# Performance work log

Measured on AMD Instinct MI355X. Metric: run time of the kernel, lower is better.

## Reference

```python
import jax, jax.numpy as jnp
import numpy as np

K, N, M, P, H = 8, 16, 8, 32, 32
BSZ, T = 128, 512
TAU = 0.5
P_STAY = 0.9


def setup_inputs() -> dict:
    key = jax.random.key(0)
    ks = jax.random.split(key, 20)
    f32 = jnp.float32
    norm = lambda k, s, sc=1.0: (jax.random.normal(k, s) * sc).astype(f32)
    sw = 1.0 / np.sqrt(H)  # torch GRU init scale
    return {
        "a_seq": norm(ks[0], (BSZ, T, P)),
        "A": norm(ks[1], (K, N, N), 0.1),
        "Bmat": norm(ks[2], (K, N, M), 0.1),
        "C": norm(ks[3], (K, P, N), 0.1),
        "Q": (jnp.tile(jnp.eye(N, dtype=f32)[None], (K, 1, 1)) + norm(ks[4], (K, N, N), 0.01)),
        "wih_f": norm(ks[5], (3 * H, P), sw),
        "whh_f": norm(ks[6], (3 * H, H), sw),
        "bih_f": norm(ks[7], (3 * H,), sw),
        "bhh_f": norm(ks[8], (3 * H,), sw),
        "wih_b": norm(ks[9], (3 * H, P), sw),
        "whh_b": norm(ks[10], (3 * H, H), sw),
        "bih_b": norm(ks[11], (3 * H,), sw),
        "bhh_b": norm(ks[12], (3 * H,), sw),
        "wl": norm(ks[13], (K * K, 2 * H), sw),
        "bl": norm(ks[14], (K * K,), sw),
        "wi": norm(ks[15], (K, 2 * H), sw),
        "bi": norm(ks[16], (K,), sw),
        "u0": jax.random.uniform(ks[17], (BSZ, K), minval=1e-6, maxval=1.0 - 1e-6, dtype=f32),
        "useq": jax.random.uniform(ks[18], (BSZ, T - 1, K), minval=1e-6, maxval=1.0 - 1e-6, dtype=f32),
    }


def _gru_dir(gx, whh, bhh, reverse):
    # gx: [T, B, 3H] precomputed input-to-hidden gates; torch GRU cell math
    def step(h, g):
        gh = h @ whh.T + bhh
        xr, xz, xn = jnp.split(g, 3, axis=-1)
        hr, hz, hn = jnp.split(gh, 3, axis=-1)
        r = jax.nn.sigmoid(xr + hr)
        z = jax.nn.sigmoid(xz + hz)
        n = jnp.tanh(xn + r * hn)
        h_new = (1.0 - z) * n + z * h
        return h_new, h_new
    h0 = jnp.zeros((gx.shape[1], whh.shape[1]), gx.dtype)
    _, hs = jax.lax.scan(step, h0, gx, reverse=reverse)
    return hs  # [T, B, H]


def reference(a_seq, A, Bmat, C, Q, wih_f, whh_f, bih_f, bhh_f,
              wih_b, whh_b, bih_b, bhh_b, wl, bl, wi, bi, u0, useq):
    Bn, Tn, _ = a_seq.shape
    Kn = A.shape[0]
    x = a_seq.transpose(1, 0, 2)  # [T, B, P]
    hf = _gru_dir(x @ wih_f.T + bih_f, whh_f, bhh_f, False)
    hb = _gru_dir(x @ wih_b.T + bih_b, whh_b, bhh_b, True)
    h_seq = jnp.concatenate([hf, hb], axis=-1)  # [T, B, 2H]

    logits = (h_seq @ wl.T + bl).reshape(Tn, Bn, Kn, Kn)  # [T, B, K, K]
    init_logits = h_seq[0] @ wi.T + bi                     # [B, K]

    g0 = -jnp.log(-jnp.log(u0))
    gseq = -jnp.log(-jnp.log(useq))  # [B, T-1, K]

    # t = 0 (soft gumbel-softmax since is_training=True)
    y0 = jax.nn.softmax((init_logits + g0) / TAU, axis=-1)
    lq0 = (y0 * jax.nn.log_softmax(init_logits, axis=-1)).sum(-1)
    lp0 = (y0 * jnp.log(1.0 / Kn)).sum(-1)  # torch: full_like(1/K).log()

    trans = jnp.full((Kn, Kn), (1.0 - P_STAY) / (Kn - 1), a_seq.dtype)
    trans = trans.at[jnp.arange(Kn), jnp.arange(Kn)].set(P_STAY)

    def step(y_prev, xs):
        lg, g = xs  # lg: [B, K, K], g: [B, K]
        l_t = jnp.einsum('bk,bkj->bj', y_prev, lg)
        y_t = jax.nn.softmax((l_t + g) / TAU, axis=-1)
        lq = (y_t * jax.nn.log_softmax(l_t, axis=-1)).sum(-1)
        tp = y_prev @ trans
        lp = (y_t * jnp.log(jnp.clip(tp, 1e-8))).sum(-1)
        return y_t, (y_t, lq, lp)

    _, (ys, lqs, lps) = jax.lax.scan(step, y0, (logits[1:], gseq.transpose(1, 0, 2)))

    y_seq = jnp.concatenate([y0[None], ys], axis=0).transpose(1, 0, 2)  # [B, T, K]
    log_qseq = jnp.concatenate([lq0[None], lqs], axis=0).T              # [B, T]
    log_pseq = jnp.concatenate([lp0[None], lps], axis=0).T              # [B, T]

    A_seq = jnp.einsum('btk,kij->btij', y_seq, A)
    B_seq = jnp.einsum('btk,knm->btnm', y_seq, Bmat)
    Q_seq = jnp.einsum('btk,kij->btij', y_seq, Q)
    C_seq = jnp.broadcast_to(C[0], (Bn, Tn) + C[0].shape)
    return (A_seq, B_seq, C_seq, Q_seq, log_qseq, log_pseq)
```

## Files before the change

kernel.cpp:

```cpp
#include <hip/hip_runtime.h>
#include <math.h>

#define T 512
#define B 128
#define KK 8
#define HH 32
#define PP 32

#define WS_GX    0
#define WS_GS    6291456
#define WS_HSEQ  12582912
#define WS_LOGITS 0
#define WS_INIT  16777216
#define WS_YSEQ  16778240

#define OUT_A    0
#define OUT_B    16777216
#define OUT_C    25165824
#define OUT_Q    58720256
#define OUT_LQ   75497472
#define OUT_LP   75563008

#define TINV 2.0f
#define PSTAY 0.9f
#define OFFV (0.1f / 7.0f)
#define DPS (PSTAY - OFFV)
#define LOG_INV_K (-2.0794415416798357f)

typedef float f4v __attribute__((ext_vector_type(4)));
typedef __attribute__((address_space(3))) float as3f;

__device__ __forceinline__ void dma16(unsigned ldsbyte, int voffbyte, const void* sbase) {
    asm volatile("s_mov_b32 m0, %0\n\t"
                 "global_load_lds_dwordx4 %1, %2"
                 :: "s"(ldsbyte), "v"(voffbyte), "s"(sbase)
                 : "memory");
}
__device__ __forceinline__ void st16(void* p, f4v v) {
    asm volatile("global_store_dwordx4 %0, %1, off" :: "v"(p), "v"(v) : "memory");
}
__device__ __forceinline__ f4v ldsr16(int addr) {
    f4v out;
    asm volatile("ds_read_b128 %0, %1" : "=v"(out) : "v"(addr));
    return out;
}
__device__ __forceinline__ f4v ldg16(const void* p) {
    f4v out;
    asm volatile("global_load_dwordx4 %0, %1, off" : "=v"(out) : "v"(p) : "memory");
    return out;
}
__device__ __forceinline__ float ldg4(const void* p) {
    float out;
    asm volatile("global_load_dword %0, %1, off" : "=v"(out) : "v"(p) : "memory");
    return out;
}

__global__ __launch_bounds__(192) void gx_kernel(
    const float* __restrict__ a_seq,
    const float* __restrict__ wih_f, const float* __restrict__ bih_f,
    const float* __restrict__ wih_b, const float* __restrict__ bih_b,
    float* __restrict__ gx) {
    __shared__ float xt[64 * 32];
    int blk = blockIdx.x;
    int b = blk >> 3;
    int t0 = (blk & 7) << 6;
    int g = threadIdx.x;
    int dir = (g >= 96) ? 1 : 0;
    int gg = dir ? (g - 96) : g;
    const float* w = dir ? wih_b : wih_f;
    const float* bv = dir ? bih_b : bih_f;

    {
        const float4* src = (const float4*)(a_seq + ((size_t)b * T + t0) * PP);
        float4* dst = (float4*)xt;
        for (int idx = g; idx < 512; idx += 192) dst[idx] = src[idx];
    }
    float wreg[32];
#pragma unroll
    for (int q = 0; q < 8; ++q) {
        float4 wv = *(const float4*)(w + (size_t)gg * PP + q * 4);
        wreg[q * 4 + 0] = wv.x; wreg[q * 4 + 1] = wv.y;
        wreg[q * 4 + 2] = wv.z; wreg[q * 4 + 3] = wv.w;
    }
    float bias = bv[gg];
    __syncthreads();

    float* op = gx + ((size_t)(dir * B + b) * T + t0) * 96 + gg;
#pragma unroll 4
    for (int r = 0; r < 64; ++r) {
        const float4* xr = (const float4*)(xt + r * 32);
        float acc = bias;
#pragma unroll
        for (int q = 0; q < 8; ++q) {
            float4 xv = xr[q];
            acc = fmaf(xv.x, wreg[q * 4 + 0], acc);
            acc = fmaf(xv.y, wreg[q * 4 + 1], acc);
            acc = fmaf(xv.z, wreg[q * 4 + 2], acc);
            acc = fmaf(xv.w, wreg[q * 4 + 3], acc);
        }
        op[(size_t)r * 96] = acc;
    }
}

__global__ __launch_bounds__(64, 1) void gru_kernel(
    const float* __restrict__ gx,
    const float* __restrict__ whh_f, const float* __restrict__ bhh_f,
    const float* __restrict__ whh_b, const float* __restrict__ bhh_b,
    float* __restrict__ hseq) {
    int cid = blockIdx.x;
    int b = cid & 127;
    int dir = cid >> 7;
    int i = threadIdx.x & 31;
    const float* whh = dir ? whh_b : whh_f;
    const float* bhh = dir ? bhh_b : bhh_f;
    const float* gp0 = gx + (size_t)cid * (T * 96);

    f4v wr[8], wz[8], wn[8];
#pragma unroll
    for (int q = 0; q < 8; ++q) {
        wr[q] = ldg16(whh + (size_t)i * 32 + q * 4);
        wz[q] = ldg16(whh + (size_t)(32 + i) * 32 + q * 4);
        wn[q] = ldg16(whh + (size_t)(64 + i) * 32 + q * 4);
    }
    float bhr = ldg4(bhh + i);
    float bhz = ldg4(bhh + 32 + i);
    float bhn = ldg4(bhh + 64 + i);

    const float* p = gp0 + (dir ? (T - 1) * 96 : 0);
    int gstep = dir ? -96 : 96;
    int voff = (((dir ? (T - 1) : 0) * B + b) * 64 + dir * 32 + i) * 4;
    int vstep = dir ? -(B * 64 * 4) : (B * 64 * 4);

    float pxrA[8], pxzA[8], pxnA[8], pxrB[8], pxzB[8], pxnB[8];

#define LOADG(PR, PZ, PN, G0) do {                                             \
        _Pragma("unroll")                                                      \
        for (int u_ = 0; u_ < 8; ++u_) {                                       \
            int sc_ = (G0) * 8 + u_; if (sc_ > T - 1) sc_ = T - 1;             \
            const float* rp_ = p + sc_ * gstep;                                \
            PR[u_] = ldg4(rp_ + i);                                            \
            PZ[u_] = ldg4(rp_ + 32 + i);                                       \
            PN[u_] = ldg4(rp_ + 64 + i);                                       \
        }                                                                      \
    } while (0)

#define GWAIT(N) do {                                                          \
        asm volatile("s_waitcnt vmcnt(" #N ")" ::: "memory");                  \
        __builtin_amdgcn_sched_barrier(0);                                     \
    } while (0)

#define GSTEP(PR, PZ, PN, SLOT) do {                                           \
        float hr_ = PR[SLOT] + bhr;                                            \
        float hz_ = PZ[SLOT] + bhz;                                            \
        float hn_ = bhn;                                                       \
        _Pragma("unroll")                                                      \
        for (int q_ = 0; q_ < 8; ++q_) {                                       \
            _Pragma("unroll")                                                  \
            for (int c_ = 0; c_ < 4; ++c_) {                                   \
                float hj_ = __uint_as_float(                                   \
                    __builtin_amdgcn_readlane(__float_as_uint(h), q_ * 4 + c_)); \
                hr_ = fmaf(wr[q_][c_], hj_, hr_);                              \
                hz_ = fmaf(wz[q_][c_], hj_, hz_);                              \
                hn_ = fmaf(wn[q_][c_], hj_, hn_);                              \
            }                                                                  \
        }                                                                      \
        float r_ = __builtin_amdgcn_rcpf(1.f + __expf(-hr_));                  \
        float z_ = __builtin_amdgcn_rcpf(1.f + __expf(-hz_));                  \
        float na_ = fmaf(r_, hn_, PN[SLOT]);                                   \
        float e2_ = __expf(-2.f * fabsf(na_));                                 \
        float n_ = copysignf((1.f - e2_) * __builtin_amdgcn_rcpf(1.f + e2_), na_); \
        h = fmaf(z_, h - n_, n_);                                              \
        asm volatile("global_store_dword %0, %1, %2"                           \
                     :: "v"(voff), "v"(h), "s"(hseq) : "memory");              \
        voff += vstep;                                                         \
    } while (0)

    LOADG(pxrA, pxzA, pxnA, 0);
    GWAIT(0);
    float h = 0.f;

    for (int gq = 0; gq < 32; ++gq) {
        LOADG(pxrB, pxzB, pxnB, 2 * gq + 1);
        GWAIT(32);
        GSTEP(pxrA, pxzA, pxnA, 0); GSTEP(pxrA, pxzA, pxnA, 1);
        GSTEP(pxrA, pxzA, pxnA, 2); GSTEP(pxrA, pxzA, pxnA, 3);
        GSTEP(pxrA, pxzA, pxnA, 4); GSTEP(pxrA, pxzA, pxnA, 5);
        GSTEP(pxrA, pxzA, pxnA, 6); GSTEP(pxrA, pxzA, pxnA, 7);
        LOADG(pxrA, pxzA, pxnA, 2 * gq + 2);
        GWAIT(32);
        GSTEP(pxrB, pxzB, pxnB, 0); GSTEP(pxrB, pxzB, pxnB, 1);
        GSTEP(pxrB, pxzB, pxnB, 2); GSTEP(pxrB, pxzB, pxnB, 3);
        GSTEP(pxrB, pxzB, pxnB, 4); GSTEP(pxrB, pxzB, pxnB, 5);
        GSTEP(pxrB, pxzB, pxnB, 6); GSTEP(pxrB, pxzB, pxnB, 7);
    }
#undef LOADG
#undef GWAIT
#undef GSTEP
}

__global__ __launch_bounds__(256) void logits_kernel(
    const float* __restrict__ hseq,
    const float* __restrict__ wl, const float* __restrict__ bl,
    const float* __restrict__ wi, const float* __restrict__ bi,
    float* __restrict__ logits, float* __restrict__ initl) {
    __shared__ float wls[64 * 65];
    __shared__ float hrow[4][64];
    int tid = threadIdx.x;
    for (int i2 = tid; i2 < 1024; i2 += 256) {
        float4 v = ((const float4*)wl)[i2];
        int gr = i2 >> 4;
        int cc = (i2 & 15) * 4;
        float* d = &wls[gr * 65 + cc];
        d[0] = v.x; d[1] = v.y; d[2] = v.z; d[3] = v.w;
    }
    int q = tid >> 6;
    int tb = blockIdx.x * 4 + q;
    int g = tid & 63;
    hrow[q][g] = hseq[(size_t)tb * 64 + g];
    __syncthreads();
    float acc = bl[g];
    const float* wrow = &wls[g * 65];
#pragma unroll
    for (int c = 0; c < 64; ++c) acc = fmaf(wrow[c], hrow[q][c], acc);
    logits[(size_t)tb * 64 + g] = acc * TINV;
    if (tb < B && g < 8) {
        float a2 = bi[g];
        const float* w2 = wi + (size_t)g * 64;
#pragma unroll
        for (int c = 0; c < 64; ++c) a2 = fmaf(w2[c], hrow[q][c], a2);
        initl[tb * 8 + g] = a2;
    }
}

__global__ __launch_bounds__(256) void gsc_kernel(
    const float* __restrict__ u0, const float* __restrict__ useq,
    float* __restrict__ gs) {
    int id = blockIdx.x * 256 + threadIdx.x;
    if (id >= T * B * KK) return;
    int j = id & 7;
    int b = (id >> 3) & 127;
    int t = id >> 10;
    float u = (t == 0) ? u0[b * 8 + j]
                       : useq[((size_t)b * (T - 1) + (t - 1)) * 8 + j];
    gs[id] = -logf(-logf(u)) * TINV;
}

__global__ __launch_bounds__(128, 1) void scan_kernel(
    const float* __restrict__ logits, const float* __restrict__ initl,
    const float* __restrict__ gs, float* __restrict__ yseq) {
    __shared__ float lds[6][2304];
    int tid = threadIdx.x;
    int wave = tid >> 6;
    int r = tid & 63;
    int b0 = blockIdx.x * 32;
    int b = b0 + (r & 31);
    int k15 = r & 15;

    unsigned ldsU = (unsigned)(unsigned long long)(as3f*)(&lds[0][0]);

#define ISSUE(tt, sl) do {                                                   \
        unsigned lb_ = ldsU + (unsigned)((sl) * 9216);                       \
        const char* bt_ = (const char*)logits + (size_t)(tt) * 32768;        \
        const char* gt_ = (const char*)gs + (size_t)(tt) * 4096;             \
        dma16(lb_ + 0 * 1024u, lof[0], bt_);                                 \
        dma16(lb_ + 1 * 1024u, lof[1], bt_);                                 \
        dma16(lb_ + 2 * 1024u, lof[2], bt_);                                 \
        dma16(lb_ + 3 * 1024u, lof[3], bt_);                                 \
        dma16(lb_ + 4 * 1024u, lof[4], bt_);                                 \
        dma16(lb_ + 5 * 1024u, lof[5], bt_);                                 \
        dma16(lb_ + 6 * 1024u, lof[6], bt_);                                 \
        dma16(lb_ + 7 * 1024u, lof[7], bt_);                                 \
        dma16(lb_ + 8192u, gof, gt_);                                        \
    } while (0)

    if (wave == 1) {
        int lof[8];
#pragma unroll
        for (int q = 0; q < 8; ++q) {
            int rr = q * 4 + (r >> 4);
            int cc = r & 15;
            lof[q] = (((b0 + rr) * 64) + ((cc ^ (rr & 15)) << 2)) << 2;
        }
        int gof;
        {
            int rg = r >> 1;
            int cc = r & 1;
            gof = (((b0 + rg) * 8) + ((cc ^ (rg & 1)) << 2)) << 2;
        }
#pragma unroll
        for (int p = 1; p <= 5; ++p) ISSUE(p, p);
        asm volatile("s_waitcnt vmcnt(36)" ::: "memory");
        __builtin_amdgcn_s_barrier();
        for (int t = 1; t < T; ++t) {
            asm volatile("s_waitcnt vmcnt(27)" ::: "memory");
            __builtin_amdgcn_s_barrier();
            int tp = t + 5; if (tp > T - 1) tp = T - 1;
            ISSUE(tp, (t + 5) % 6);
        }
        return;
    }

    unsigned rbase = ldsU + (unsigned)((r & 31) * 256);
    unsigned gbase = ldsU + 8192u + (unsigned)((r & 31) * 32);

#define SREAD(LL, GA, GB, tt) do {                                           \
        int so_ = ((tt) % 6) * 9216;                                         \
        _Pragma("unroll")                                                    \
        for (int m_ = 0; m_ < 16; ++m_)                                      \
            LL[m_] = ldsr16((int)(rbase + so_ + ((m_ ^ k15) << 4)));         \
        GA = ldsr16((int)(gbase + so_ + ((r & 1) << 4)));                    \
        GB = ldsr16((int)(gbase + so_ + (((r & 1) ^ 1) << 4)));              \
    } while (0)

#define LWAIT() do {                                                         \
        asm volatile("s_waitcnt lgkmcnt(0)" ::: "memory");                   \
        __builtin_amdgcn_sched_barrier(0);                                   \
    } while (0)

#define SCOMP(LL, GA, GB, tt) do {                                           \
        float pl_[8];                                                        \
        _Pragma("unroll")                                                    \
        for (int j_ = 0; j_ < 8; ++j_) pl_[j_] = 0.f;                        \
        _Pragma("unroll")                                                    \
        for (int k_ = 0; k_ < 8; ++k_) {                                     \
            f4v w0_ = LL[2 * k_], w1_ = LL[2 * k_ + 1];                      \
            float ek_ = e[k_];                                               \
            pl_[0] = fmaf(ek_, w0_.x, pl_[0]); pl_[1] = fmaf(ek_, w0_.y, pl_[1]); \
            pl_[2] = fmaf(ek_, w0_.z, pl_[2]); pl_[3] = fmaf(ek_, w0_.w, pl_[3]); \
            pl_[4] = fmaf(ek_, w1_.x, pl_[4]); pl_[5] = fmaf(ek_, w1_.y, pl_[5]); \
            pl_[6] = fmaf(ek_, w1_.z, pl_[6]); pl_[7] = fmaf(ek_, w1_.w, pl_[7]); \
        }                                                                    \
        float gg_[8] = {GA.x, GA.y, GA.z, GA.w, GB.x, GB.y, GB.z, GB.w};     \
        float ss_ = 0.f;                                                     \
        _Pragma("unroll")                                                    \
        for (int j_ = 0; j_ < 8; ++j_) {                                     \
            float a_ = fmaf(pl_[j_], sinv, gg_[j_]);                         \
            e[j_] = __expf(a_);                                              \
            ss_ += e[j_];                                                    \
        }                                                                    \
        sinv = __builtin_amdgcn_rcpf(ss_);                                   \
        if (r < 32) {                                                        \
            f4v v0_ = (f4v){e[0] * sinv, e[1] * sinv, e[2] * sinv, e[3] * sinv}; \
            f4v v1_ = (f4v){e[4] * sinv, e[5] * sinv, e[6] * sinv, e[7] * sinv}; \
            st16(&yp[2 * (tt)], v0_);                                        \
            st16(&yp[2 * (tt) + 1], v1_);                                    \
        }                                                                    \
    } while (0)

    f4v* yp = (f4v*)(yseq + (size_t)b * T * 8);
    float e[8];
    float sinv;

    {
        const f4v* il4 = (const f4v*)(initl + b * 8);
        f4v i0 = il4[0], i1 = il4[1];
        const f4v* g4 = (const f4v*)(gs + b * 8);
        f4v G0 = g4[0], G1 = g4[1];
        float a[8];
        a[0] = fmaf(i0.x, TINV, G0.x); a[1] = fmaf(i0.y, TINV, G0.y);
        a[2] = fmaf(i0.z, TINV, G0.z); a[3] = fmaf(i0.w, TINV, G0.w);
        a[4] = fmaf(i1.x, TINV, G1.x); a[5] = fmaf(i1.y, TINV, G1.y);
        a[6] = fmaf(i1.z, TINV, G1.z); a[7] = fmaf(i1.w, TINV, G1.w);
        float ssum = 0.f;
#pragma unroll
        for (int j = 0; j < 8; ++j) { e[j] = __expf(a[j]); ssum += e[j]; }
        sinv = __builtin_amdgcn_rcpf(ssum);
        if (r < 32) {
            f4v y0v = (f4v){e[0] * sinv, e[1] * sinv, e[2] * sinv, e[3] * sinv};
            f4v y1v = (f4v){e[4] * sinv, e[5] * sinv, e[6] * sinv, e[7] * sinv};
            st16(&yp[0], y0v);
            st16(&yp[1], y1v);
        }
    }

    f4v LA[16], LB[16], gaA, gbA, gaB, gbB;

    __builtin_amdgcn_s_barrier();
    SREAD(LA, gaA, gbA, 1);

    for (int t = 1; t < T - 1; t += 2) {
        __builtin_amdgcn_s_barrier();
        LWAIT();
        SREAD(LB, gaB, gbB, t + 1);
        SCOMP(LA, gaA, gbA, t);

        __builtin_amdgcn_s_barrier();
        LWAIT();
        SREAD(LA, gaA, gbA, t + 2);
        SCOMP(LB, gaB, gbB, t + 1);
    }
    __builtin_amdgcn_s_barrier();
    LWAIT();
    SCOMP(LA, gaA, gbA, T - 1);
#undef ISSUE
#undef SREAD
#undef LWAIT
#undef SCOMP
}

__global__ __launch_bounds__(256) void lqlp_kernel(
    const float* __restrict__ logits, const float* __restrict__ initl,
    const float* __restrict__ yseq,
    float* __restrict__ logq, float* __restrict__ logp) {
    int tid = blockIdx.x * 256 + threadIdx.x;
    if (tid >= B * T) return;
    int b = tid >> 9;
    int t = tid & (T - 1);

    const float4* yt4 = (const float4*)(yseq + (size_t)tid * 8);
    float4 y0 = yt4[0], y1 = yt4[1];
    float yt[8] = {y0.x, y0.y, y0.z, y0.w, y1.x, y1.y, y1.z, y1.w};

    float l[8];
    float lp;
    if (t == 0) {
        const float4* il4 = (const float4*)(initl + b * 8);
        float4 i0 = il4[0], i1 = il4[1];
        l[0] = i0.x; l[1] = i0.y; l[2] = i0.z; l[3] = i0.w;
        l[4] = i1.x; l[5] = i1.y; l[6] = i1.z; l[7] = i1.w;
        float sy = ((yt[0] + yt[1]) + (yt[2] + yt[3])) + ((yt[4] + yt[5]) + (yt[6] + yt[7]));
        lp = LOG_INV_K * sy;
    } else {
        const float4* yp4 = (const float4*)(yseq + (size_t)tid * 8 - 8);
        float4 p0 = yp4[0], p1 = yp4[1];
        float ypv[8] = {p0.x, p0.y, p0.z, p0.w, p1.x, p1.y, p1.z, p1.w};
        const float4* L4 = (const float4*)(logits + ((size_t)t * B + b) * 64);
#pragma unroll
        for (int j = 0; j < 8; ++j) l[j] = 0.f;
#pragma unroll
        for (int k = 0; k < 8; ++k) {
            float4 w0 = L4[2 * k], w1 = L4[2 * k + 1];
            float yk = ypv[k];
            l[0] = fmaf(yk, w0.x, l[0]); l[1] = fmaf(yk, w0.y, l[1]);
            l[2] = fmaf(yk, w0.z, l[2]); l[3] = fmaf(yk, w0.w, l[3]);
            l[4] = fmaf(yk, w1.x, l[4]); l[5] = fmaf(yk, w1.y, l[5]);
            l[6] = fmaf(yk, w1.z, l[6]); l[7] = fmaf(yk, w1.w, l[7]);
        }
#pragma unroll
        for (int j = 0; j < 8; ++j) l[j] *= 0.5f;
        float sy = ((ypv[0] + ypv[1]) + (ypv[2] + ypv[3])) + ((ypv[4] + ypv[5]) + (ypv[6] + ypv[7]));
        float acc = 0.f;
#pragma unroll
        for (int j = 0; j < 8; ++j) {
            float tp = fmaf(DPS, ypv[j], OFFV * sy);
            acc = fmaf(yt[j], logf(fmaxf(tp, 1e-8f)), acc);
        }
        lp = acc;
    }
    float m = fmaxf(fmaxf(fmaxf(l[0], l[1]), fmaxf(l[2], l[3])),
                    fmaxf(fmaxf(l[4], l[5]), fmaxf(l[6], l[7])));
    float se = 0.f;
#pragma unroll
    for (int j = 0; j < 8; ++j) se += __expf(l[j] - m);
    float lse = m + logf(se);
    float lq = 0.f;
#pragma unroll
    for (int j = 0; j < 8; ++j) lq = fmaf(yt[j], l[j] - lse, lq);
    logq[tid] = lq;
    logp[tid] = lp;
}

__global__ __launch_bounds__(256) void out_kernel(
    const float* __restrict__ yseq,
    const float* __restrict__ A, const float* __restrict__ Bm,
    const float* __restrict__ C, const float* __restrict__ Q,
    float4* __restrict__ out4) {
    __shared__ float tab[6144];
    int tid = threadIdx.x;
    int bt0 = blockIdx.x * 64;
    {
        float4* t4 = (float4*)tab;
        const float4* A4 = (const float4*)A;
        const float4* B4 = (const float4*)Bm;
        const float4* Q4 = (const float4*)Q;
        const float4* C4 = (const float4*)C;
        for (int i2 = tid; i2 < 512; i2 += 256) t4[i2] = A4[i2];
        if (tid < 256) t4[512 + tid] = B4[tid];
        for (int i2 = tid; i2 < 512; i2 += 256) t4[768 + i2] = Q4[i2];
        if (tid < 128) t4[1280 + tid] = C4[tid];
        const float4* Y4 = (const float4*)(yseq + (size_t)bt0 * 8);
        if (tid < 128) t4[1408 + tid] = Y4[tid];
    }
    __syncthreads();

    int wave = tid >> 6;
    int lane = tid & 63;
    const float4* t4 = (const float4*)tab;

    if (wave == 0 || wave == 1) {
        int tbase = (wave == 0) ? 0 : 768;
        size_t obase = (wave == 0) ? (size_t)(OUT_A / 4) : (size_t)(OUT_Q / 4);
        float4 wreg[8];
#pragma unroll
        for (int k = 0; k < 8; ++k) wreg[k] = t4[tbase + k * 64 + lane];
        for (int bt = 0; bt < 64; ++bt) {
            float4 ya = t4[1408 + bt * 2];
            float4 yb = t4[1408 + bt * 2 + 1];
            float yk[8] = {ya.x, ya.y, ya.z, ya.w, yb.x, yb.y, yb.z, yb.w};
            float4 v = make_float4(0.f, 0.f, 0.f, 0.f);
#pragma unroll
            for (int k = 0; k < 8; ++k) {
                v.x = fmaf(yk[k], wreg[k].x, v.x);
                v.y = fmaf(yk[k], wreg[k].y, v.y);
                v.z = fmaf(yk[k], wreg[k].z, v.z);
                v.w = fmaf(yk[k], wreg[k].w, v.w);
            }
            out4[obase + (size_t)(bt0 + bt) * 64 + lane] = v;
        }
    } else if (wave == 2) {
        if (lane < 32) {
            float4 wreg[8];
#pragma unroll
            for (int k = 0; k < 8; ++k) wreg[k] = t4[512 + k * 32 + lane];
            for (int bt = 0; bt < 64; ++bt) {
                float4 ya = t4[1408 + bt * 2];
                float4 yb = t4[1408 + bt * 2 + 1];
                float yk[8] = {ya.x, ya.y, ya.z, ya.w, yb.x, yb.y, yb.z, yb.w};
                float4 v = make_float4(0.f, 0.f, 0.f, 0.f);
#pragma unroll
                for (int k = 0; k < 8; ++k) {
                    v.x = fmaf(yk[k], wreg[k].x, v.x);
                    v.y = fmaf(yk[k], wreg[k].y, v.y);
                    v.z = fmaf(yk[k], wreg[k].z, v.z);
                    v.w = fmaf(yk[k], wreg[k].w, v.w);
                }
                out4[(size_t)(OUT_B / 4) + (size_t)(bt0 + bt) * 32 + lane] = v;
            }
        } else {
            float4 c0 = t4[1280 + (lane - 32)];
            for (int bt = 0; bt < 64; ++bt)
                out4[(size_t)(OUT_C / 4) + (size_t)(bt0 + bt) * 128 + (lane - 32)] = c0;
        }
    } else {
        float4 c1 = t4[1280 + 32 + lane];
        float4 c2 = (lane < 32) ? t4[1280 + 96 + lane] : make_float4(0.f, 0.f, 0.f, 0.f);
        for (int bt = 0; bt < 64; ++bt) {
            out4[(size_t)(OUT_C / 4) + (size_t)(bt0 + bt) * 128 + 32 + lane] = c1;
            if (lane < 32)
                out4[(size_t)(OUT_C / 4) + (size_t)(bt0 + bt) * 128 + 96 + lane] = c2;
        }
    }
}

extern "C" void kernel_launch(void* const* d_in, const int* in_sizes, int n_in,
                              void* d_out, int out_size, void* d_ws, size_t ws_size,
                              hipStream_t stream) {
    const float* a_seq = (const float*)d_in[0];
    const float* A     = (const float*)d_in[1];
    const float* Bmat  = (const float*)d_in[2];
    const float* C     = (const float*)d_in[3];
    const float* Q     = (const float*)d_in[4];
    const float* wih_f = (const float*)d_in[5];
    const float* whh_f = (const float*)d_in[6];
    const float* bih_f = (const float*)d_in[7];
    const float* bhh_f = (const float*)d_in[8];
    const float* wih_b = (const float*)d_in[9];
    const float* whh_b = (const float*)d_in[10];
    const float* bih_b = (const float*)d_in[11];
    const float* bhh_b = (const float*)d_in[12];
    const float* wl    = (const float*)d_in[13];
    const float* bl    = (const float*)d_in[14];
    const float* wi    = (const float*)d_in[15];
    const float* bi    = (const float*)d_in[16];
    const float* u0    = (const float*)d_in[17];
    const float* useq  = (const float*)d_in[18];

    float* ws = (float*)d_ws;
    float* gx     = ws + WS_GX;
    float* gsb    = ws + WS_GS;
    float* hseq   = ws + WS_HSEQ;
    float* logits = ws + WS_LOGITS;
    float* initl  = ws + WS_INIT;
    float* yseq   = ws + WS_YSEQ;

    float* outf = (float*)d_out;
    float* logq = outf + OUT_LQ;
    float* logp = outf + OUT_LP;

    gx_kernel<<<B * (T / 64), 192, 0, stream>>>(a_seq, wih_f, bih_f, wih_b, bih_b, gx);
    gru_kernel<<<256, 64, 0, stream>>>(gx, whh_f, bhh_f, whh_b, bhh_b, hseq);
    {
        int total = B * T * KK;
        gsc_kernel<<<(total + 255) / 256, 256, 0, stream>>>(u0, useq, gsb);
    }
    logits_kernel<<<T * B / 4, 256, 0, stream>>>(hseq, wl, bl, wi, bi, logits, initl);
    scan_kernel<<<4, 128, 0, stream>>>(logits, initl, gsb, yseq);
    lqlp_kernel<<<(B * T + 255) / 256, 256, 0, stream>>>(logits, initl, yseq, logq, logp);
    out_kernel<<<B * T / 64, 256, 0, stream>>>(yseq, A, Bmat, C, Q, (float4*)d_out);
}
```

Measured before the change: 485.9 us.

## Hoist GRU readlanes ahead of FMAs; split lqlp rows across 8 lanes

In the GRU step, all 32 hidden-state broadcasts via readlane are issued up front, with a sched barrier, before the FMA chains, so the scalar readlane latency is not interleaved with the dependent math. The lqlp kernel now gives each (b,t) row to 8 lanes. Each lane loads one logits row slice and the rows are combined with xor shuffles, instead of one thread doing all 64 loads serially. This adds more threads, redundant per-lane softmax and log work, and shuffle overhead.

Result: no change. 487.2 us (+0.3%).

```diff
diff --git a/kernel.cpp b/kernel.cpp
--- a/kernel.cpp
+++ b/kernel.cpp
@@ -150,6 +150,12 @@
     } while (0)
 
 #define GSTEP(PR, PZ, PN, SLOT) do {                                           \
+        float hj_[32];                                                         \
+        _Pragma("unroll")                                                      \
+        for (int jj = 0; jj < 32; ++jj)                                        \
+            hj_[jj] = __uint_as_float(                                         \
+                __builtin_amdgcn_readlane(__float_as_uint(h), jj));            \
+        __builtin_amdgcn_sched_barrier(0);                                     \
         float hr_ = PR[SLOT] + bhr;                                            \
         float hz_ = PZ[SLOT] + bhz;                                            \
         float hn_ = bhn;                                                       \
@@ -157,11 +163,10 @@
         for (int q_ = 0; q_ < 8; ++q_) {                                       \
             _Pragma("unroll")                                                  \
             for (int c_ = 0; c_ < 4; ++c_) {                                   \
-                float hj_ = __uint_as_float(                                   \
-                    __builtin_amdgcn_readlane(__float_as_uint(h), q_ * 4 + c_)); \
-                hr_ = fmaf(wr[q_][c_], hj_, hr_);                              \
-                hz_ = fmaf(wz[q_][c_], hj_, hz_);                              \
-                hn_ = fmaf(wn[q_][c_], hj_, hn_);                              \
+                float hjv_ = hj_[q_ * 4 + c_];                                 \
+                hr_ = fmaf(wr[q_][c_], hjv_, hr_);                             \
+                hz_ = fmaf(wz[q_][c_], hjv_, hz_);                             \
+                hn_ = fmaf(wn[q_][c_], hjv_, hn_);                             \
             }                                                                  \
         }                                                                      \
         float r_ = __builtin_amdgcn_rcpf(1.f + __expf(-hr_));                  \
@@ -403,13 +408,14 @@
     const float* __restrict__ yseq,
     float* __restrict__ logq, float* __restrict__ logp) {
     int tid = blockIdx.x * 256 + threadIdx.x;
-    if (tid >= B * T) return;
-    int b = tid >> 9;
-    int t = tid & (T - 1);
-
-    const float4* yt4 = (const float4*)(yseq + (size_t)tid * 8);
-    float4 y0 = yt4[0], y1 = yt4[1];
-    float yt[8] = {y0.x, y0.y, y0.z, y0.w, y1.x, y1.y, y1.z, y1.w};
+    int j = tid & 7;
+    int row = tid >> 3;
+    int b = row >> 9;
+    int t = row & (T - 1);
+
+    const float4* yt4 = (const float4*)(yseq + (size_t)row * 8);
+    float4 ya = yt4[0], yb = yt4[1];
+    float yt[8] = {ya.x, ya.y, ya.z, ya.w, yb.x, yb.y, yb.z, yb.w};
 
     float l[8];
     float lp;
@@ -421,29 +427,27 @@
         float sy = ((yt[0] + yt[1]) + (yt[2] + yt[3])) + ((yt[4] + yt[5]) + (yt[6] + yt[7]));
         lp = LOG_INV_K * sy;
     } else {
-        const float4* yp4 = (const float4*)(yseq + (size_t)tid * 8 - 8);
+        const float4* yp4 = (const float4*)(yseq + (size_t)row * 8 - 8);
         float4 p0 = yp4[0], p1 = yp4[1];
         float ypv[8] = {p0.x, p0.y, p0.z, p0.w, p1.x, p1.y, p1.z, p1.w};
-        const float4* L4 = (const float4*)(logits + ((size_t)t * B + b) * 64);
-#pragma unroll
-        for (int j = 0; j < 8; ++j) l[j] = 0.f;
-#pragma unroll
-        for (int k = 0; k < 8; ++k) {
-            float4 w0 = L4[2 * k], w1 = L4[2 * k + 1];
-            float yk = ypv[k];
-            l[0] = fmaf(yk, w0.x, l[0]); l[1] = fmaf(yk, w0.y, l[1]);
-            l[2] = fmaf(yk, w0.z, l[2]); l[3] = fmaf(yk, w0.w, l[3]);
-            l[4] = fmaf(yk, w1.x, l[4]); l[5] = fmaf(yk, w1.y, l[5]);
-            l[6] = fmaf(yk, w1.z, l[6]); l[7] = fmaf(yk, w1.w, l[7]);
-        }
-#pragma unroll
-        for (int j = 0; j < 8; ++j) l[j] *= 0.5f;
+        float ypj = yseq[(size_t)row * 8 - 8 + j];
+        const float4* L4 = (const float4*)(logits + ((size_t)t * B + b) * 64 + j * 8);
+        float4 r0 = L4[0], r1 = L4[1];
+        float c[8] = {ypj * r0.x, ypj * r0.y, ypj * r0.z, ypj * r0.w,
+                      ypj * r1.x, ypj * r1.y, ypj * r1.z, ypj * r1.w};
+#pragma unroll
+        for (int s = 1; s <= 4; s <<= 1) {
+#pragma unroll
+            for (int m = 0; m < 8; ++m) c[m] += __shfl_xor(c[m], s, 64);
+        }
+#pragma unroll
+        for (int m = 0; m < 8; ++m) l[m] = c[m] * 0.5f;
         float sy = ((ypv[0] + ypv[1]) + (ypv[2] + ypv[3])) + ((ypv[4] + ypv[5]) + (ypv[6] + ypv[7]));
         float acc = 0.f;
 #pragma unroll
-        for (int j = 0; j < 8; ++j) {
-            float tp = fmaf(DPS, ypv[j], OFFV * sy);
-            acc = fmaf(yt[j], logf(fmaxf(tp, 1e-8f)), acc);
+        for (int m = 0; m < 8; ++m) {
+            float tp = fmaf(DPS, ypv[m], OFFV * sy);
+            acc = fmaf(yt[m], logf(fmaxf(tp, 1e-8f)), acc);
         }
         lp = acc;
     }
@@ -451,13 +455,15 @@
                     fmaxf(fmaxf(l[4], l[5]), fmaxf(l[6], l[7])));
     float se = 0.f;
 #pragma unroll
-    for (int j = 0; j < 8; ++j) se += __expf(l[j] - m);
+    for (int m2 = 0; m2 < 8; ++m2) se += __expf(l[m2] - m);
     float lse = m + logf(se);
     float lq = 0.f;
 #pragma unroll
-    for (int j = 0; j < 8; ++j) lq = fmaf(yt[j], l[j] - lse, lq);
-    logq[tid] = lq;
-    logp[tid] = lp;
+    for (int m2 = 0; m2 < 8; ++m2) lq = fmaf(yt[m2], l[m2] - lse, lq);
+    if (j == 0) {
+        logq[row] = lq;
+        logp[row] = lp;
+    }
 }
 
 __global__ __launch_bounds__(256) void out_kernel(
@@ -585,6 +591,6 @@
     }
     logits_kernel<<<T * B / 4, 256, 0, stream>>>(hseq, wl, bl, wi, bi, logits, initl);
     scan_kernel<<<4, 128, 0, stream>>>(logits, initl, gsb, yseq);
-    lqlp_kernel<<<(B * T + 255) / 256, 256, 0, stream>>>(logits, initl, yseq, logq, logp);
+    lqlp_kernel<<<B * T * KK / 256, 256, 0, stream>>>(logits, initl, yseq, logq, logp);
     out_kernel<<<B * T / 64, 256, 0, stream>>>(yseq, A, Bmat, C, Q, (float4*)d_out);
 }
```
